# Kernel optimization log

Measured on AMD Instinct MI355X. Metric: run time of the kernel, lower is better.

Reference implementation:

```python
import jax, jax.numpy as jnp
import numpy as np

D_MODEL = 1024
N_HEADS = 16
N_KV = 4
HEAD_DIM = D_MODEL // N_HEADS
B, T, CACHE_LEN = 2, 1024, 1024
MAX_SEQ = 4096
ROPE_BASE = 10000.0


def _rope_tables(max_seq_len=MAX_SEQ, head_dim=HEAD_DIM, base=ROPE_BASE):
    inv_freq = 1.0 / (base ** (np.arange(0, head_dim, 2, dtype=np.float32) / head_dim))
    t = np.arange(max_seq_len, dtype=np.float32)
    freqs = np.outer(t, inv_freq)                      # [S, hd/2]
    emb = np.concatenate([freqs, freqs], axis=-1)      # [S, hd]
    return jnp.asarray(np.cos(emb)), jnp.asarray(np.sin(emb))


def _rotate_half(x):
    x1, x2 = jnp.split(x, 2, axis=-1)
    return jnp.concatenate([-x2, x1], axis=-1)


def setup_inputs() -> dict:
    key = jax.random.key(0)
    ks = jax.random.split(key, 8)
    return {
        "x": jax.random.normal(ks[0], (B, T, D_MODEL), dtype=jnp.float32),
        "k_cache": jax.random.normal(ks[1], (B, N_KV, CACHE_LEN, HEAD_DIM), dtype=jnp.float32),
        "v_cache": jax.random.normal(ks[2], (B, N_KV, CACHE_LEN, HEAD_DIM), dtype=jnp.float32),
        "position_indices": jax.random.randint(ks[3], (B, T), 0, 1024, dtype=jnp.int32),
        "Wq": jax.random.normal(ks[4], (D_MODEL, D_MODEL), dtype=jnp.float32) * 0.02,
        "Wk": jax.random.normal(ks[5], (D_MODEL, N_KV * HEAD_DIM), dtype=jnp.float32) * 0.02,
        "Wv": jax.random.normal(ks[6], (D_MODEL, N_KV * HEAD_DIM), dtype=jnp.float32) * 0.02,
        "Wo": jax.random.normal(ks[7], (D_MODEL, D_MODEL), dtype=jnp.float32) * 0.02,
    }


def reference(x, k_cache, v_cache, position_indices, Wq, Wk, Wv, Wo):
    Bq, Tq, C = x.shape
    n_kv, cache_len, hd = k_cache.shape[1], k_cache.shape[2], k_cache.shape[3]
    n_heads = Wq.shape[1] // hd
    n_rep = n_heads // n_kv
    scale = hd ** -0.5

    cos, sin = _rope_tables()

    # projections -> [B, H, T, hd]
    q = (x @ Wq).reshape(Bq, Tq, n_heads, hd).transpose(0, 2, 1, 3)
    k = (x @ Wk).reshape(Bq, Tq, n_kv, hd).transpose(0, 2, 1, 3)
    v = (x @ Wv).reshape(Bq, Tq, n_kv, hd).transpose(0, 2, 1, 3)

    # progress-aware RoPE: position-indexed gather into tables, offset by cache len
    offset = cache_len
    t_seq = jnp.arange(Tq, dtype=jnp.int32)[None, :] + offset          # [1, T]
    idx = jnp.clip(position_indices.astype(jnp.int32) + t_seq, 0, cos.shape[0] - 1)  # [B, T]
    cos_b = cos[idx][:, None]  # [B, 1, T, hd]
    sin_b = sin[idx][:, None]
    q = q * cos_b + _rotate_half(q) * sin_b
    k = k * cos_b + _rotate_half(k) * sin_b

    # KV-cache concat
    k = jnp.concatenate([k_cache, k], axis=2)  # [B, n_kv, S, hd]
    v = jnp.concatenate([v_cache, v], axis=2)

    # GQA head expansion (repeat each kv head n_rep times, contiguous grouping)
    k_exp = jnp.repeat(k, n_rep, axis=1)  # [B, H, S, hd]
    v_exp = jnp.repeat(v, n_rep, axis=1)

    # manual attention path (k_cache provided -> NO causal mask, matching torch code)
    attn = jnp.einsum("bhtd,bhsd->bhts", q, k_exp) * scale
    attn = jax.nn.softmax(attn, axis=-1)
    out = jnp.einsum("bhts,bhsd->bhtd", attn, v_exp)
    out = out.transpose(0, 2, 1, 3).reshape(Bq, Tq, C)
    return out @ Wo, k, v
```

## Files before the change

### kernel.cpp

```cpp
#include <hip/hip_runtime.h>
#include <hip/hip_bf16.h>
#include <stdint.h>

#define D_MODEL 1024
#define N_HEADS 16
#define N_KV 4
#define HD 64
#define BB 2
#define TT 1024
#define CACHE_LEN 1024
#define SS 2048
#define MAX_SEQ 4096
#define QKV_N 1536
#define GRP_EL (SS * HD)

typedef __attribute__((ext_vector_type(8))) short bf16x8;
typedef __attribute__((ext_vector_type(4))) float f32x4;

__device__ inline short f2bs(float f) {
    __hip_bfloat16 h = __float2bfloat16(f);
    return *reinterpret_cast<short*>(&h);
}

#define GLDS(gp, lp) __builtin_amdgcn_global_load_lds( \
    (const __attribute__((address_space(1))) void*)(gp), \
    (__attribute__((address_space(3))) void*)(lp), 16, 0, 0)

__device__ inline int kfrag_off(int s, int d) {
    return (s >> 4) * 1024 + ((d >= 32) ? 512 : 0) + ((((d & 31) >> 3) * 16 + (s & 15)) * 8) + (d & 7);
}
__device__ inline int vfrag_off(int s, int d) {
    return ((s >> 5) * 4 + (d >> 4)) * 512 + ((((s >> 2) & 3) * 16 + (d & 15)) * 8)
         + (((s >> 4) & 1) * 4) + (s & 3);
}

__device__ void transp_body(const float* __restrict__ src, short* __restrict__ dst,
                            int N, int bx, int by) {
    __shared__ short tile[32][34];
    int tx = threadIdx.x & 31, ty = threadIdx.x >> 5;
    int n0 = bx * 32, k0 = by * 32;
#pragma unroll
    for (int i = 0; i < 4; i++)
        tile[ty + i * 8][tx] = f2bs(src[(size_t)(k0 + ty + i * 8) * N + n0 + tx]);
    __syncthreads();
#pragma unroll
    for (int i = 0; i < 4; i++)
        dst[(size_t)(n0 + ty + i * 8) * 1024 + k0 + tx] = tile[tx][ty + i * 8];
}

__global__ void k_prep(const float* __restrict__ x, short* __restrict__ xb,
                       const float* __restrict__ Wq, const float* __restrict__ Wk,
                       const float* __restrict__ Wv, const float* __restrict__ Wo,
                       short* __restrict__ Wt, short* __restrict__ Wot,
                       const float* __restrict__ k_cache, const float* __restrict__ v_cache,
                       float* __restrict__ k_out, float* __restrict__ v_out,
                       short* __restrict__ kf, short* __restrict__ vf,
                       const int* __restrict__ pos,
                       float* __restrict__ costab, float* __restrict__ sintab) {
    int id = blockIdx.x;
    int g = threadIdx.x;
    if (id < 2048) {
        int i = (id * 256 + g) * 4;
        float4 v = *reinterpret_cast<const float4*>(x + i);
        short4 o = make_short4(f2bs(v.x), f2bs(v.y), f2bs(v.z), f2bs(v.w));
        *reinterpret_cast<short4*>(xb + i) = o;
        return;
    }
    id -= 2048;
    if (id < 1024) { transp_body(Wq, Wt, 1024, id & 31, id >> 5); return; }
    id -= 1024;
    if (id < 256)  { transp_body(Wk, Wt + (size_t)1024 * 1024, 256, id & 7, id >> 3); return; }
    id -= 256;
    if (id < 256)  { transp_body(Wv, Wt + (size_t)1280 * 1024, 256, id & 7, id >> 3); return; }
    id -= 256;
    if (id < 1024) { transp_body(Wo, Wot, 1024, id & 31, id >> 5); return; }
    id -= 1024;
    if (id < 2048) {
        int i = id * 256 + g;
        int d = i & 63;
        int s = (i >> 6) & 1023;
        int bh = i >> 16;
        size_t cidx = ((size_t)bh * CACHE_LEN + s) * HD + d;
        size_t oidx = ((size_t)bh * SS + s) * HD + d;
        float kv = k_cache[cidx];
        float vv = v_cache[cidx];
        k_out[oidx] = kv;
        v_out[oidx] = vv;
        kf[(size_t)bh * GRP_EL + kfrag_off(s, d)] = f2bs(kv);
        vf[(size_t)bh * GRP_EL + vfrag_off(s, d)] = f2bs(vv);
        return;
    }
    id -= 2048;
    {
        int p = id * 256 + g;
        int row = p >> 5, i = p & 31;
        int idx = pos[row] + (row & 1023) + CACHE_LEN;
        idx = min(max(idx, 0), MAX_SEQ - 1);
        float inv = expf(-(float)i * (9.210340371976184f / 32.0f));
        float sv, cv;
        sincosf((float)idx * inv, &sv, &cv);
        costab[p] = cv;
        sintab[p] = sv;
    }
}

__global__ __launch_bounds__(256) void k_gemm_qkv(
    const short* __restrict__ A, const short* __restrict__ Bt,
    const float* __restrict__ costab, const float* __restrict__ sintab,
    short* __restrict__ qb, short* __restrict__ kf, short* __restrict__ vf,
    float* __restrict__ k_out, float* __restrict__ v_out) {
    __shared__ short smem[16384];
    short* sA = smem;
    short* sB = smem + 8192;
    float* eplds = (float*)smem;
    int m0 = blockIdx.y * 64, n0 = blockIdx.x * 64;
    int g = threadIdx.x;
    int lane = g & 63, wave = g >> 6;
    int wr = wave >> 1, wc = wave & 1;
    int quad = lane >> 4, l15 = lane & 15;

    f32x4 acc[2][2] = {};

    int srow = (lane >> 2);
    int scol = (lane & 3) * 8;
#define STAGE_G(buf, k0)                                                              \
    {                                                                                 \
        _Pragma("unroll")                                                             \
        for (int i = 0; i < 2; i++) {                                                 \
            int cb = wave * 2 + i;                                                    \
            int h = cb >> 2, c = cb & 3;                                              \
            int row = c * 16 + srow;                                                  \
            int kcol = (k0) + h * 32 + scol;                                          \
            GLDS(A + (size_t)(m0 + row) * 1024 + kcol,                                \
                 (char*)(sA + (buf) * 4096 + h * 2048) + c * 1024);                   \
            GLDS(Bt + (size_t)(n0 + row) * 1024 + kcol,                               \
                 (char*)(sB + (buf) * 4096 + h * 2048) + c * 1024);                   \
        }                                                                             \
    }

    STAGE_G(0, 0);
    __syncthreads();
    int buf = 0;
    for (int k0 = 0; k0 < 1024; k0 += 64) {
        if (k0 + 64 < 1024) STAGE_G(buf ^ 1, k0 + 64);
#pragma unroll
        for (int h = 0; h < 2; h++) {
            bf16x8 af[2], bfr[2];
#pragma unroll
            for (int i = 0; i < 2; i++)
                af[i] = *reinterpret_cast<const bf16x8*>(
                    sA + buf * 4096 + h * 2048 + (wr * 32 + i * 16 + l15) * 32 + quad * 8);
#pragma unroll
            for (int j = 0; j < 2; j++)
                bfr[j] = *reinterpret_cast<const bf16x8*>(
                    sB + buf * 4096 + h * 2048 + (wc * 32 + j * 16 + l15) * 32 + quad * 8);
#pragma unroll
            for (int i = 0; i < 2; i++)
#pragma unroll
                for (int j = 0; j < 2; j++)
                    acc[i][j] = __builtin_amdgcn_mfma_f32_16x16x32_bf16(af[i], bfr[j], acc[i][j], 0, 0, 0);
        }
        __syncthreads();
        buf ^= 1;
    }
#pragma unroll
    for (int i = 0; i < 2; i++)
#pragma unroll
        for (int j = 0; j < 2; j++)
#pragma unroll
            for (int r = 0; r < 4; r++)
                eplds[(wr * 32 + i * 16 + quad * 4 + r) * 65 + wc * 32 + j * 16 + l15] = acc[i][j][r];
    __syncthreads();

    int bx = blockIdx.x;
    const float QS = 0.18033688011112042f;
    if (bx < 20) {
#pragma unroll
        for (int rep = 0; rep < 8; rep++) {
            int p = rep * 256 + g;
            int row = p >> 5, i = p & 31;
            int m = m0 + row;
            int b = m >> 10, t = m & 1023;
            float cv = costab[m * 32 + i], sv = sintab[m * 32 + i];
            float x1 = eplds[row * 65 + i], x2 = eplds[row * 65 + i + 32];
            float o1 = x1 * cv - x2 * sv;
            float o2 = x2 * cv + x1 * sv;
            if (bx < 16) {
                size_t qbase = ((size_t)(b * N_HEADS + bx) * TT + t) * HD;
                qb[qbase + i]      = f2bs(o1 * QS);
                qb[qbase + i + 32] = f2bs(o2 * QS);
            } else {
                int h = bx - 16;
                int s = CACHE_LEN + t;
                size_t kbase = ((size_t)(b * N_KV + h) * SS + s) * HD;
                k_out[kbase + i]      = o1;
                k_out[kbase + i + 32] = o2;
                short* kfb = kf + (size_t)(b * N_KV + h) * GRP_EL;
                kfb[kfrag_off(s, i)]      = f2bs(o1);
                kfb[kfrag_off(s, i + 32)] = f2bs(o2);
            }
        }
    } else {
        int h = bx - 20;
#pragma unroll
        for (int rep = 0; rep < 16; rep++) {
            int p = rep * 256 + g;
            int row = p >> 6, d = p & 63;
            int m = m0 + row;
            int b = m >> 10, t = m & 1023;
            int s = CACHE_LEN + t;
            float val = eplds[row * 65 + d];
            v_out[((size_t)(b * N_KV + h) * SS + s) * HD + d] = val;
            vf[(size_t)(b * N_KV + h) * GRP_EL + vfrag_off(s, d)] = f2bs(val);
        }
    }
}

__global__ __launch_bounds__(256) void k_gemm64(
    const short* __restrict__ A, const short* __restrict__ Bt, float* __restrict__ C,
    int M, int N, int K) {
    __shared__ short sA[2][2][2048];
    __shared__ short sB[2][2][2048];
    int m0 = blockIdx.y * 64, n0 = blockIdx.x * 64;
    int g = threadIdx.x;
    int lane = g & 63, wave = g >> 6;
    int wr = wave >> 1, wc = wave & 1;
    int quad = lane >> 4, l15 = lane & 15;

    f32x4 acc[2][2] = {};
    int srow = (lane >> 2);
    int scol = (lane & 3) * 8;
#define STAGE_W(buf, k0)                                                             \
    {                                                                                \
        _Pragma("unroll")                                                            \
        for (int i = 0; i < 2; i++) {                                                \
            int cb = wave * 2 + i;                                                   \
            int h = cb >> 2, c = cb & 3;                                             \
            int row = c * 16 + srow;                                                 \
            int kcol = (k0) + h * 32 + scol;                                         \
            GLDS(A + (size_t)(m0 + row) * K + kcol, (char*)&sA[buf][h][0] + c * 1024);\
            GLDS(Bt + (size_t)(n0 + row) * K + kcol, (char*)&sB[buf][h][0] + c * 1024);\
        }                                                                            \
    }
    STAGE_W(0, 0);
    __syncthreads();
    int buf = 0;
    for (int k0 = 0; k0 < K; k0 += 64) {
        if (k0 + 64 < K) STAGE_W(buf ^ 1, k0 + 64);
#pragma unroll
        for (int h = 0; h < 2; h++) {
            bf16x8 af[2], bfr[2];
#pragma unroll
            for (int i = 0; i < 2; i++)
                af[i] = *reinterpret_cast<const bf16x8*>(&sA[buf][h][(wr * 32 + i * 16 + l15) * 32 + quad * 8]);
#pragma unroll
            for (int j = 0; j < 2; j++)
                bfr[j] = *reinterpret_cast<const bf16x8*>(&sB[buf][h][(wc * 32 + j * 16 + l15) * 32 + quad * 8]);
#pragma unroll
            for (int i = 0; i < 2; i++)
#pragma unroll
                for (int j = 0; j < 2; j++)
                    acc[i][j] = __builtin_amdgcn_mfma_f32_16x16x32_bf16(af[i], bfr[j], acc[i][j], 0, 0, 0);
        }
        __syncthreads();
        buf ^= 1;
    }
#pragma unroll
    for (int i = 0; i < 2; i++) {
        int m = m0 + wr * 32 + i * 16 + quad * 4;
#pragma unroll
        for (int j = 0; j < 2; j++) {
            int n = n0 + wc * 32 + j * 16 + l15;
#pragma unroll
            for (int r = 0; r < 4; r++)
                C[(size_t)(m + r) * N + n] = acc[i][j][r];
        }
    }
}

__global__ __launch_bounds__(256, 4) void k_attn(
    const short* __restrict__ qb, const short* __restrict__ kf, const short* __restrict__ vf,
    short* __restrict__ ob) {
    __shared__ short tile[2][8192];
    int bh = blockIdx.x;
    int b = bh >> 4, h = bh & 15;
    int hkv = h >> 2;
    int lane = threadIdx.x & 63, wave = threadIdx.x >> 6;
    int quad = lane >> 4, l15 = lane & 15;
    int tw0 = blockIdx.y * 128 + wave * 16;
    int tw1 = tw0 + 64;

    const short* qrow0 = qb + ((size_t)bh * TT + tw0 + l15) * HD;
    const short* qrow1 = qb + ((size_t)bh * TT + tw1 + l15) * HD;
    bf16x8 aq00 = *reinterpret_cast<const bf16x8*>(qrow0 + quad * 8);
    bf16x8 aq01 = *reinterpret_cast<const bf16x8*>(qrow0 + 32 + quad * 8);
    bf16x8 aq10 = *reinterpret_cast<const bf16x8*>(qrow1 + quad * 8);
    bf16x8 aq11 = *reinterpret_cast<const bf16x8*>(qrow1 + 32 + quad * 8);

    const short* kfb = kf + (size_t)(b * N_KV + hkv) * GRP_EL;
    const short* vfb = vf + (size_t)(b * N_KV + hkv) * GRP_EL;

    f32x4 o0[4] = {}, o1[4] = {};
    float lr0 = 0.f, lr1 = 0.f;

#define STAGE_KV(bufi, s0)                                                    \
    {                                                                         \
        _Pragma("unroll")                                                     \
        for (int i = 0; i < 4; i++) {                                         \
            int ch = wave * 4 + i;                                            \
            const short* src = (ch < 8)                                       \
                ? kfb + ((s0) >> 4) * 1024 + ch * 512 + lane * 8              \
                : vfb + ((s0) >> 5) * 2048 + (ch - 8) * 512 + lane * 8;       \
            GLDS(src, (char*)&tile[bufi][0] + ch * 1024);                     \
        }                                                                     \
    }

    STAGE_KV(0, 0);
    __syncthreads();
    int buf = 0;
    for (int s0 = 0; s0 < SS; s0 += 64) {
        if (s0 + 64 < SS) STAGE_KV(buf ^ 1, s0 + 64);
        const short* tb = &tile[buf][0];
#pragma unroll
        for (int pp = 0; pp < 2; pp++) {
            f32x4 s0c[2], s1c[2];
#pragma unroll
            for (int ti = 0; ti < 2; ti++) {
                int nt = pp * 2 + ti;
                bf16x8 ak0 = *reinterpret_cast<const bf16x8*>(tb + nt * 1024 + lane * 8);
                bf16x8 ak1 = *reinterpret_cast<const bf16x8*>(tb + nt * 1024 + 512 + lane * 8);
                f32x4 z = {};
                z = __builtin_amdgcn_mfma_f32_16x16x32_bf16(ak0, aq00, z, 0, 0, 0);
                z = __builtin_amdgcn_mfma_f32_16x16x32_bf16(ak1, aq01, z, 0, 0, 0);
                s0c[ti] = z;
                f32x4 w = {};
                w = __builtin_amdgcn_mfma_f32_16x16x32_bf16(ak0, aq10, w, 0, 0, 0);
                w = __builtin_amdgcn_mfma_f32_16x16x32_bf16(ak1, aq11, w, 0, 0, 0);
                s1c[ti] = w;
            }
            bf16x8 bp0, bp1;
#pragma unroll
            for (int ti = 0; ti < 2; ti++)
#pragma unroll
                for (int r = 0; r < 4; r++) {
                    float p0 = exp2f(s0c[ti][r]);
                    float p1 = exp2f(s1c[ti][r]);
                    lr0 += p0;
                    lr1 += p1;
                    bp0[ti * 4 + r] = f2bs(p0);
                    bp1[ti * 4 + r] = f2bs(p1);
                }
#pragma unroll
            for (int dt = 0; dt < 4; dt++) {
                bf16x8 av = *reinterpret_cast<const bf16x8*>(
                    tb + 4096 + (pp * 4 + dt) * 512 + lane * 8);
                o0[dt] = __builtin_amdgcn_mfma_f32_16x16x32_bf16(av, bp0, o0[dt], 0, 0, 0);
                o1[dt] = __builtin_amdgcn_mfma_f32_16x16x32_bf16(av, bp1, o1[dt], 0, 0, 0);
            }
        }
        __syncthreads();
        buf ^= 1;
    }

    lr0 += __shfl_xor(lr0, 16);
    lr0 += __shfl_xor(lr0, 32);
    lr1 += __shfl_xor(lr1, 16);
    lr1 += __shfl_xor(lr1, 32);
    float inv0 = 1.0f / lr0;
    float inv1 = 1.0f / lr1;

    size_t row0 = (size_t)(b * TT) + tw0 + l15;
    size_t row1 = (size_t)(b * TT) + tw1 + l15;
#pragma unroll
    for (int dt = 0; dt < 4; dt++) {
        short4 w0 = make_short4(f2bs(o0[dt][0] * inv0), f2bs(o0[dt][1] * inv0),
                                f2bs(o0[dt][2] * inv0), f2bs(o0[dt][3] * inv0));
        short4 w1 = make_short4(f2bs(o1[dt][0] * inv1), f2bs(o1[dt][1] * inv1),
                                f2bs(o1[dt][2] * inv1), f2bs(o1[dt][3] * inv1));
        *reinterpret_cast<short4*>(ob + row0 * D_MODEL + h * 64 + dt * 16 + quad * 4) = w0;
        *reinterpret_cast<short4*>(ob + row1 * D_MODEL + h * 64 + dt * 16 + quad * 4) = w1;
    }
}

extern "C" void kernel_launch(void* const* d_in, const int* in_sizes, int n_in,
                              void* d_out, int out_size, void* d_ws, size_t ws_size,
                              hipStream_t stream) {
    (void)in_sizes; (void)n_in; (void)out_size; (void)ws_size;
    const float* x       = (const float*)d_in[0];
    const float* k_cache = (const float*)d_in[1];
    const float* v_cache = (const float*)d_in[2];
    const int*   pos     = (const int*)d_in[3];
    const float* Wq      = (const float*)d_in[4];
    const float* Wk      = (const float*)d_in[5];
    const float* Wv      = (const float*)d_in[6];
    const float* Wo      = (const float*)d_in[7];

    float* out   = (float*)d_out;
    float* k_out = out + (size_t)BB * TT * D_MODEL;
    float* v_out = k_out + (size_t)BB * N_KV * SS * HD;

    char* ws = (char*)d_ws;
    short* xb     = (short*)(ws);
    short* Wt     = (short*)(ws + (4u << 20));
    float* costab = (float*)(ws + (7u << 20));
    float* sintab = (float*)(ws + (7u << 20) + (256u << 10));
    short* qbuf   = (short*)(ws + (8u << 20));
    short* kfr    = (short*)(ws + (12u << 20));
    short* vfr    = (short*)(ws + (14u << 20));
    short* obuf   = (short*)(ws + (16u << 20));
    short* Wot    = (short*)(ws + (20u << 20));

    k_prep<<<6912, 256, 0, stream>>>(x, xb, Wq, Wk, Wv, Wo, Wt, Wot,
                                     k_cache, v_cache, k_out, v_out, kfr, vfr,
                                     pos, costab, sintab);

    k_gemm_qkv<<<dim3(QKV_N / 64, 2048 / 64), 256, 0, stream>>>(
        xb, Wt, costab, sintab, qbuf, kfr, vfr, k_out, v_out);

    k_attn<<<dim3(32, TT / 128), 256, 0, stream>>>(qbuf, kfr, vfr, obuf);

    k_gemm64<<<dim3(1024 / 64, 2048 / 64), 256, 0, stream>>>(
        obuf, Wot, (float*)d_out, 2048, 1024, 1024);
}
```

Baseline: 148.2 us.

## Move Wo transpose and KV-cache copy into QKV GEMM launch as extra blocks

Moves the Wo transpose and the KV-cache copy/fragment packing out of the prep kernel and runs them as extra blocks of the QKV GEMM launch, which becomes a 1D grid of 768 GEMM tiles plus 3072 side-work blocks. The side work only needs to finish before attention, so it can overlap with the GEMM instead of delaying its start. The prep kernel gets smaller, but the GEMM launch now mixes two kinds of blocks, which may affect scheduling and tail behaviour. The transpose's shared tile is now passed in explicitly and reuses the GEMM's shared memory.

```diff
diff --git a/kernel.cpp b/kernel.cpp
--- a/kernel.cpp
+++ b/kernel.cpp
@@ -34,29 +34,25 @@
          + (((s >> 4) & 1) * 4) + (s & 3);
 }
 
-__device__ void transp_body(const float* __restrict__ src, short* __restrict__ dst,
-                            int N, int bx, int by) {
-    __shared__ short tile[32][34];
+__device__ void transp_body(short* __restrict__ tile, const float* __restrict__ src,
+                            short* __restrict__ dst, int N, int bx, int by) {
     int tx = threadIdx.x & 31, ty = threadIdx.x >> 5;
     int n0 = bx * 32, k0 = by * 32;
 #pragma unroll
     for (int i = 0; i < 4; i++)
-        tile[ty + i * 8][tx] = f2bs(src[(size_t)(k0 + ty + i * 8) * N + n0 + tx]);
+        tile[(ty + i * 8) * 34 + tx] = f2bs(src[(size_t)(k0 + ty + i * 8) * N + n0 + tx]);
     __syncthreads();
 #pragma unroll
     for (int i = 0; i < 4; i++)
-        dst[(size_t)(n0 + ty + i * 8) * 1024 + k0 + tx] = tile[tx][ty + i * 8];
+        dst[(size_t)(n0 + ty + i * 8) * 1024 + k0 + tx] = tile[tx * 34 + ty + i * 8];
 }
 
 __global__ void k_prep(const float* __restrict__ x, short* __restrict__ xb,
                        const float* __restrict__ Wq, const float* __restrict__ Wk,
-                       const float* __restrict__ Wv, const float* __restrict__ Wo,
-                       short* __restrict__ Wt, short* __restrict__ Wot,
-                       const float* __restrict__ k_cache, const float* __restrict__ v_cache,
-                       float* __restrict__ k_out, float* __restrict__ v_out,
-                       short* __restrict__ kf, short* __restrict__ vf,
+                       const float* __restrict__ Wv, short* __restrict__ Wt,
                        const int* __restrict__ pos,
                        float* __restrict__ costab, float* __restrict__ sintab) {
+    __shared__ short tile[32 * 34];
     int id = blockIdx.x;
     int g = threadIdx.x;
     if (id < 2048) {
@@ -67,16 +63,40 @@
         return;
     }
     id -= 2048;
-    if (id < 1024) { transp_body(Wq, Wt, 1024, id & 31, id >> 5); return; }
+    if (id < 1024) { transp_body(tile, Wq, Wt, 1024, id & 31, id >> 5); return; }
     id -= 1024;
-    if (id < 256)  { transp_body(Wk, Wt + (size_t)1024 * 1024, 256, id & 7, id >> 3); return; }
+    if (id < 256)  { transp_body(tile, Wk, Wt + (size_t)1024 * 1024, 256, id & 7, id >> 3); return; }
     id -= 256;
-    if (id < 256)  { transp_body(Wv, Wt + (size_t)1280 * 1024, 256, id & 7, id >> 3); return; }
+    if (id < 256)  { transp_body(tile, Wv, Wt + (size_t)1280 * 1024, 256, id & 7, id >> 3); return; }
     id -= 256;
-    if (id < 1024) { transp_body(Wo, Wot, 1024, id & 31, id >> 5); return; }
-    id -= 1024;
-    if (id < 2048) {
-        int i = id * 256 + g;
+    {
+        int p = id * 256 + g;
+        int row = p >> 5, i = p & 31;
+        int idx = pos[row] + (row & 1023) + CACHE_LEN;
+        idx = min(max(idx, 0), MAX_SEQ - 1);
+        float inv = expf(-(float)i * (9.210340371976184f / 32.0f));
+        float sv, cv;
+        sincosf((float)idx * inv, &sv, &cv);
+        costab[p] = cv;
+        sintab[p] = sv;
+    }
+}
+
+__global__ __launch_bounds__(256) void k_gemm_qkv(
+    const short* __restrict__ A, const short* __restrict__ Bt,
+    const float* __restrict__ costab, const float* __restrict__ sintab,
+    short* __restrict__ qb, short* __restrict__ kf, short* __restrict__ vf,
+    float* __restrict__ k_out, float* __restrict__ v_out,
+    const float* __restrict__ Wo, short* __restrict__ Wot,
+    const float* __restrict__ k_cache, const float* __restrict__ v_cache) {
+    __shared__ short smem[16384];
+    int id = blockIdx.x;
+    int g = threadIdx.x;
+    if (id >= 768) {
+        int hid = id - 768;
+        if (hid < 1024) { transp_body(smem, Wo, Wot, 1024, hid & 31, hid >> 5); return; }
+        hid -= 1024;
+        int i = hid * 256 + g;
         int d = i & 63;
         int s = (i >> 6) & 1023;
         int bh = i >> 16;
@@ -90,37 +110,16 @@
         vf[(size_t)bh * GRP_EL + vfrag_off(s, d)] = f2bs(vv);
         return;
     }
-    id -= 2048;
-    {
-        int p = id * 256 + g;
-        int row = p >> 5, i = p & 31;
-        int idx = pos[row] + (row & 1023) + CACHE_LEN;
-        idx = min(max(idx, 0), MAX_SEQ - 1);
-        float inv = expf(-(float)i * (9.210340371976184f / 32.0f));
-        float sv, cv;
-        sincosf((float)idx * inv, &sv, &cv);
-        costab[p] = cv;
-        sintab[p] = sv;
-    }
-}
-
-__global__ __launch_bounds__(256) void k_gemm_qkv(
-    const short* __restrict__ A, const short* __restrict__ Bt,
-    const float* __restrict__ costab, const float* __restrict__ sintab,
-    short* __restrict__ qb, short* __restrict__ kf, short* __restrict__ vf,
-    float* __restrict__ k_out, float* __restrict__ v_out) {
-    __shared__ short smem[16384];
     short* sA = smem;
     short* sB = smem + 8192;
     float* eplds = (float*)smem;
-    int m0 = blockIdx.y * 64, n0 = blockIdx.x * 64;
-    int g = threadIdx.x;
+    int bxg = id % 24, byg = id / 24;
+    int m0 = byg * 64, n0 = bxg * 64;
     int lane = g & 63, wave = g >> 6;
     int wr = wave >> 1, wc = wave & 1;
     int quad = lane >> 4, l15 = lane & 15;
 
     f32x4 acc[2][2] = {};
-
     int srow = (lane >> 2);
     int scol = (lane & 3) * 8;
 #define STAGE_G(buf, k0)                                                              \
@@ -137,7 +136,6 @@
                  (char*)(sB + (buf) * 4096 + h * 2048) + c * 1024);                   \
         }                                                                             \
     }
-
     STAGE_G(0, 0);
     __syncthreads();
     int buf = 0;
@@ -172,9 +170,8 @@
                 eplds[(wr * 32 + i * 16 + quad * 4 + r) * 65 + wc * 32 + j * 16 + l15] = acc[i][j][r];
     __syncthreads();
 
-    int bx = blockIdx.x;
     const float QS = 0.18033688011112042f;
-    if (bx < 20) {
+    if (bxg < 20) {
 #pragma unroll
         for (int rep = 0; rep < 8; rep++) {
             int p = rep * 256 + g;
@@ -185,12 +182,12 @@
             float x1 = eplds[row * 65 + i], x2 = eplds[row * 65 + i + 32];
             float o1 = x1 * cv - x2 * sv;
             float o2 = x2 * cv + x1 * sv;
-            if (bx < 16) {
-                size_t qbase = ((size_t)(b * N_HEADS + bx) * TT + t) * HD;
+            if (bxg < 16) {
+                size_t qbase = ((size_t)(b * N_HEADS + bxg) * TT + t) * HD;
                 qb[qbase + i]      = f2bs(o1 * QS);
                 qb[qbase + i + 32] = f2bs(o2 * QS);
             } else {
-                int h = bx - 16;
+                int h = bxg - 16;
                 int s = CACHE_LEN + t;
                 size_t kbase = ((size_t)(b * N_KV + h) * SS + s) * HD;
                 k_out[kbase + i]      = o1;
@@ -201,7 +198,7 @@
             }
         }
     } else {
-        int h = bx - 20;
+        int h = bxg - 20;
 #pragma unroll
         for (int rep = 0; rep < 16; rep++) {
             int p = rep * 256 + g;
@@ -410,12 +407,11 @@
     short* obuf   = (short*)(ws + (16u << 20));
     short* Wot    = (short*)(ws + (20u << 20));
 
-    k_prep<<<6912, 256, 0, stream>>>(x, xb, Wq, Wk, Wv, Wo, Wt, Wot,
-                                     k_cache, v_cache, k_out, v_out, kfr, vfr,
-                                     pos, costab, sintab);
-
-    k_gemm_qkv<<<dim3(QKV_N / 64, 2048 / 64), 256, 0, stream>>>(
-        xb, Wt, costab, sintab, qbuf, kfr, vfr, k_out, v_out);
+    k_prep<<<3840, 256, 0, stream>>>(x, xb, Wq, Wk, Wv, Wt, pos, costab, sintab);
+
+    k_gemm_qkv<<<3840, 256, 0, stream>>>(
+        xb, Wt, costab, sintab, qbuf, kfr, vfr, k_out, v_out,
+        Wo, Wot, k_cache, v_cache);
 
     k_attn<<<dim3(32, TT / 128), 256, 0, stream>>>(qbuf, kfr, vfr, obuf);
 
```

New measurement: 145.3 us, median of 2. No clear change (-1.9%).
